# Kernel tuning notes

Measured on AMD Instinct MI355X. Metric: run time of the kernel, lower is better.

Reference implementation:

```python
import jax, jax.numpy as jnp
import numpy as np

B = 16384
NEG = 10
V = 100000
E = 128

def setup_inputs() -> dict:
    key = jax.random.key(0)
    k1, k2, k3, k4, k5 = jax.random.split(key, 5)
    input_word = jax.random.randint(k1, (B,), 0, V)
    context_word = jax.random.randint(k2, (B,), 0, V)
    noise_words = jax.random.randint(k3, (B * NEG,), 0, V)
    # torch init: uniform_(-1, 1)
    W_in = jax.random.uniform(k4, (V, E), jnp.float32, -1.0, 1.0)
    W_ctx = jax.random.uniform(k5, (V, E), jnp.float32, -1.0, 1.0)
    return {"input_word": input_word, "context_word": context_word,
            "noise_words": noise_words, "W_in": W_in, "W_ctx": W_ctx}

def reference(input_word, context_word, noise_words, W_in, W_ctx):
    center = W_in[input_word]               # [B, E]
    ctx = W_ctx[context_word]               # [B, E]
    # positive score: per-example dot product
    out_loss = jax.nn.log_sigmoid(jnp.einsum('be,be->b', ctx, center))  # [B]
    noise = W_ctx[noise_words].reshape(B, NEG, E)                       # [B, NEG, E]
    # negative scores: -u_k . v_c
    neg_scores = -jnp.einsum('bke,be->bk', noise, center)               # [B, NEG]
    noise_loss = jax.nn.log_sigmoid(neg_scores).sum(axis=1)             # [B]
    return -(out_loss + noise_loss).mean()
```

## Files before the change

### kernel.cpp

```cpp
#include <hip/hip_runtime.h>

constexpr int kB   = 16384;
constexpr int kNeg = 10;
constexpr int kE   = 128;
constexpr int kWavesPerBlock = 4;
constexpr int kBlocks = kB / kWavesPerBlock;

__device__ __forceinline__ float log_sigmoid(float x) {
    return fminf(x, 0.0f) - log1pf(expf(-fabsf(x)));
}

__device__ __forceinline__ float dot4(float4 a, float4 b) {
    return a.x * b.x + a.y * b.y + a.z * b.z + a.w * b.w;
}

__global__ __launch_bounds__(256, 8) void w2v_loss_kernel(
    const int*   __restrict__ input_word,
    const int*   __restrict__ context_word,
    const int*   __restrict__ noise_words,
    const float* __restrict__ W_in,
    const float* __restrict__ W_ctx,
    float*       __restrict__ partials)
{
    const int tid  = threadIdx.x;
    const int wave = tid >> 6;
    const int lane = tid & 63;
    const int half = lane >> 5;
    const int l32  = lane & 31;

    const int b = __builtin_amdgcn_readfirstlane(blockIdx.x * kWavesPerBlock + wave);

    const int iw = input_word[b];
    const int cw = context_word[b];
    int nw[kNeg];
    #pragma unroll
    for (int k = 0; k < kNeg; ++k)
        nw[k] = noise_words[b * kNeg + k];

    int ridx[6];
    ridx[0] = half ? nw[5] : cw;
    #pragma unroll
    for (int j = 1; j <= 4; ++j)
        ridx[j] = half ? nw[5 + j] : nw[j - 1];
    ridx[5] = half ? cw : nw[4];

    const float4 c = ((const float4*)(W_in + (size_t)iw * kE))[l32];
    float4 r[6];
    #pragma unroll
    for (int j = 0; j < 6; ++j)
        r[j] = ((const float4*)(W_ctx + (size_t)ridx[j] * kE))[l32];

    float d[6];
    #pragma unroll
    for (int j = 0; j < 6; ++j)
        d[j] = dot4(c, r[j]);

    #pragma unroll
    for (int off = 16; off > 0; off >>= 1) {
        #pragma unroll
        for (int j = 0; j < 6; ++j)
            d[j] += __shfl_xor(d[j], off);
    }

    float v = d[0];
    #pragma unroll
    for (int j = 1; j < 6; ++j)
        v = (l32 == j) ? d[j] : v;
    const bool isPos = (half == 0) && (l32 == 0);
    v = isPos ? v : -v;
    const bool active = half ? (l32 < 5) : (l32 < 6);
    float s = active ? log_sigmoid(v) : 0.0f;

    #pragma unroll
    for (int off = 16; off > 0; off >>= 1)
        s += __shfl_xor(s, off);
    s += __shfl_xor(s, 32);

    __shared__ float smem[kWavesPerBlock];
    if (lane == 0) smem[wave] = s;
    __syncthreads();
    if (tid == 0)
        partials[blockIdx.x] = smem[0] + smem[1] + smem[2] + smem[3];
}

__global__ __launch_bounds__(256) void w2v_reduce_kernel(
    const float* __restrict__ partials,
    float*       __restrict__ out)
{
    float acc = 0.0f;
    for (int i = threadIdx.x; i < kBlocks; i += 256)
        acc += partials[i];

    #pragma unroll
    for (int off = 32; off > 0; off >>= 1)
        acc += __shfl_xor(acc, off);

    __shared__ float smem[4];
    const int lane = threadIdx.x & 63;
    const int wave = threadIdx.x >> 6;
    if (lane == 0) smem[wave] = acc;
    __syncthreads();
    if (threadIdx.x == 0) {
        const float total = smem[0] + smem[1] + smem[2] + smem[3];
        out[0] = -total / (float)kB;
    }
}

extern "C" void kernel_launch(void* const* d_in, const int* in_sizes, int n_in,
                              void* d_out, int out_size, void* d_ws, size_t ws_size,
                              hipStream_t stream) {
    const int*   input_word   = (const int*)d_in[0];
    const int*   context_word = (const int*)d_in[1];
    const int*   noise_words  = (const int*)d_in[2];
    const float* W_in         = (const float*)d_in[3];
    const float* W_ctx        = (const float*)d_in[4];
    float*       out          = (float*)d_out;
    float*       partials     = (float*)d_ws;

    w2v_loss_kernel<<<kBlocks, 256, 0, stream>>>(
        input_word, context_word, noise_words, W_in, W_ctx, partials);
    w2v_reduce_kernel<<<1, 256, 0, stream>>>(partials, out);
}
```

Measured before the change: 126.9 us.

## Invert gather by bucketing training pairs per context word via atomics

Replaces the per-example gather kernel with three steps. The first zeros a per-vocabulary counter array. The second scatters each (context or noise word, input word) pair into a fixed-capacity bucket per word using atomicAdd. The third processes each vocabulary word with a half-wave, loading its W_ctx row once and looping over its bucketed input-word rows. The aim is to reuse W_ctx rows across pairs that share a word. In exchange it adds launches and atomics, reloads a W_in row for every pair, runs serial per-word loops with load imbalance, and silently drops pairs beyond 32 per word.

```diff
diff --git a/kernel.cpp b/kernel.cpp
--- a/kernel.cpp
+++ b/kernel.cpp
@@ -1,10 +1,13 @@
 #include <hip/hip_runtime.h>
 
-constexpr int kB   = 16384;
-constexpr int kNeg = 10;
-constexpr int kE   = 128;
-constexpr int kWavesPerBlock = 4;
-constexpr int kBlocks = kB / kWavesPerBlock;
+constexpr int kB    = 16384;
+constexpr int kNeg  = 10;
+constexpr int kE    = 128;
+constexpr int kV    = 100000;
+constexpr int kCap  = 32;
+constexpr int kPairs      = kB * (kNeg + 1);
+constexpr int kMainBlocks = kV / 8;
+
 
 __device__ __forceinline__ float log_sigmoid(float x) {
     return fminf(x, 0.0f) - log1pf(expf(-fabsf(x)));
@@ -14,12 +17,38 @@
     return a.x * b.x + a.y * b.y + a.z * b.z + a.w * b.w;
 }
 
-__global__ __launch_bounds__(256, 8) void w2v_loss_kernel(
-    const int*   __restrict__ input_word,
-    const int*   __restrict__ context_word,
-    const int*   __restrict__ noise_words,
+__global__ __launch_bounds__(256) void w2v_zero_counts(int* __restrict__ cnt)
+{
+    const int i = blockIdx.x * 256 + threadIdx.x;
+    if (i < kV) cnt[i] = 0;
+}
+
+__global__ __launch_bounds__(256) void w2v_build_index(
+    const int* __restrict__ input_word,
+    const int* __restrict__ context_word,
+    const int* __restrict__ noise_words,
+    int*       __restrict__ cnt,
+    int*       __restrict__ bucket)
+{
+    const int i = blockIdx.x * 256 + threadIdx.x;
+    int w, payload;
+    if (i < kB) {
+        w = context_word[i];
+        payload = input_word[i];
+    } else {
+        const int j = i - kB;
+        w = noise_words[j];
+        payload = input_word[j / kNeg] | (int)0x80000000;
+    }
+    const int slot = atomicAdd(&cnt[w], 1);
+    if (slot < kCap) bucket[w * kCap + slot] = payload;
+}
+
+__global__ __launch_bounds__(256, 8) void w2v_main(
     const float* __restrict__ W_in,
     const float* __restrict__ W_ctx,
+    const int*   __restrict__ cnt,
+    const int*   __restrict__ bucket,
     float*       __restrict__ partials)
 {
     const int tid  = threadIdx.x;
@@ -28,59 +57,36 @@
     const int half = lane >> 5;
     const int l32  = lane & 31;
 
-    const int b = __builtin_amdgcn_readfirstlane(blockIdx.x * kWavesPerBlock + wave);
+    const int word = blockIdx.x * 8 + wave * 2 + half;
 
-    const int iw = input_word[b];
-    const int cw = context_word[b];
-    int nw[kNeg];
-    #pragma unroll
-    for (int k = 0; k < kNeg; ++k)
-        nw[k] = noise_words[b * kNeg + k];
+    int c = cnt[word];
+    c = c < kCap ? c : kCap;
 
-    int ridx[6];
-    ridx[0] = half ? nw[5] : cw;
-    #pragma unroll
-    for (int j = 1; j <= 4; ++j)
-        ridx[j] = half ? nw[5 + j] : nw[j - 1];
-    ridx[5] = half ? cw : nw[4];
-
-    const float4 c = ((const float4*)(W_in + (size_t)iw * kE))[l32];
-    float4 r[6];
-    #pragma unroll
-    for (int j = 0; j < 6; ++j)
-        r[j] = ((const float4*)(W_ctx + (size_t)ridx[j] * kE))[l32];
-
-    float d[6];
-    #pragma unroll
-    for (int j = 0; j < 6; ++j)
-        d[j] = dot4(c, r[j]);
-
-    #pragma unroll
-    for (int off = 16; off > 0; off >>= 1) {
-        #pragma unroll
-        for (int j = 0; j < 6; ++j)
-            d[j] += __shfl_xor(d[j], off);
+    float s = 0.0f;
+    if (c > 0) {
+        const float4 row = ((const float4*)(W_ctx + (size_t)word * kE))[l32];
+        for (int j = 0; j < c; ++j) {
+            const int e  = bucket[word * kCap + j];
+            const int iw = e & 0x7FFFFFFF;
+            const float4 cv = ((const float4*)(W_in + (size_t)iw * kE))[l32];
+            float d = dot4(row, cv);
+            #pragma unroll
+            for (int off = 16; off > 0; off >>= 1)
+                d += __shfl_xor(d, off);
+            const float term = log_sigmoid(e < 0 ? -d : d);
+            if (l32 == 0) s += term;
+        }
     }
 
-    float v = d[0];
-    #pragma unroll
-    for (int j = 1; j < 6; ++j)
-        v = (l32 == j) ? d[j] : v;
-    const bool isPos = (half == 0) && (l32 == 0);
-    v = isPos ? v : -v;
-    const bool active = half ? (l32 < 5) : (l32 < 6);
-    float s = active ? log_sigmoid(v) : 0.0f;
-
-    #pragma unroll
-    for (int off = 16; off > 0; off >>= 1)
-        s += __shfl_xor(s, off);
-    s += __shfl_xor(s, 32);
-
-    __shared__ float smem[kWavesPerBlock];
-    if (lane == 0) smem[wave] = s;
+    __shared__ float smem[8];
+    if (l32 == 0) smem[wave * 2 + half] = s;
     __syncthreads();
-    if (tid == 0)
-        partials[blockIdx.x] = smem[0] + smem[1] + smem[2] + smem[3];
+    if (tid == 0) {
+        float t = 0.0f;
+        #pragma unroll
+        for (int k = 0; k < 8; ++k) t += smem[k];
+        partials[blockIdx.x] = t;
+    }
 }
 
 __global__ __launch_bounds__(256) void w2v_reduce_kernel(
@@ -88,7 +94,7 @@
     float*       __restrict__ out)
 {
     float acc = 0.0f;
-    for (int i = threadIdx.x; i < kBlocks; i += 256)
+    for (int i = threadIdx.x; i < kMainBlocks; i += 256)
         acc += partials[i];
 
     #pragma unroll
@@ -115,9 +121,14 @@
     const float* W_in         = (const float*)d_in[3];
     const float* W_ctx        = (const float*)d_in[4];
     float*       out          = (float*)d_out;
-    float*       partials     = (float*)d_ws;
 
-    w2v_loss_kernel<<<kBlocks, 256, 0, stream>>>(
-        input_word, context_word, noise_words, W_in, W_ctx, partials);
+    int*   cnt      = (int*)d_ws;
+    int*   bucket   = cnt + kV;
+    float* partials = (float*)(bucket + (size_t)kV * kCap);
+
+    w2v_zero_counts<<<(kV + 255) / 256, 256, 0, stream>>>(cnt);
+    w2v_build_index<<<kPairs / 256, 256, 0, stream>>>(
+        input_word, context_word, noise_words, cnt, bucket);
+    w2v_main<<<kMainBlocks, 256, 0, stream>>>(W_in, W_ctx, cnt, bucket, partials);
     w2v_reduce_kernel<<<1, 256, 0, stream>>>(partials, out);
 }
```

After: 175.4 us. 1.38x slower.
